# Kernel tuning notes

Measured on AMD Instinct MI355X. Metric: run time of the kernel, lower is better.

## Reference

```python
import jax, jax.numpy as jnp
import numpy as np

MOMENTUM = 0.9
BN_EPS = 1e-5
NORM_EPS = 1e-12
NUM_CLASSES = 10000
DIM_MLP = 512
NUM_EXPERTS = 3
FEAT_DIM = 256
N = 4096


def _l2norm(x, axis=-1):
    # F.normalize: x / max(||x||, eps)
    n = jnp.sqrt(jnp.sum(x * x, axis=axis, keepdims=True))
    return x / jnp.maximum(n, NORM_EPS)


def setup_inputs() -> dict:
    key = jax.random.key(0)
    ks = jax.random.split(key, 8)
    feat_in = jax.random.normal(ks[0], (N, DIM_MLP * NUM_EXPERTS), dtype=jnp.float32)
    label = jax.random.randint(ks[1], (N,), 0, NUM_CLASSES, dtype=jnp.int32)
    # encoder params
    W1 = jax.random.normal(ks[2], (DIM_MLP * NUM_EXPERTS, DIM_MLP), dtype=jnp.float32) / np.sqrt(DIM_MLP * NUM_EXPERTS)
    b1 = jnp.zeros((DIM_MLP,), dtype=jnp.float32)
    gamma = jnp.ones((DIM_MLP,), dtype=jnp.float32)
    beta = jnp.zeros((DIM_MLP,), dtype=jnp.float32)
    W2 = jax.random.normal(ks[3], (DIM_MLP, FEAT_DIM), dtype=jnp.float32) / np.sqrt(DIM_MLP)
    b2 = jnp.zeros((FEAT_DIM,), dtype=jnp.float32)
    # memory bank buffer: randn then row-normalized (as in __init__)
    memory_pt = _l2norm(jax.random.normal(ks[4], (NUM_CLASSES, FEAT_DIM), dtype=jnp.float32))
    return {"feat_in": feat_in, "label": label, "W1": W1, "b1": b1,
            "gamma": gamma, "beta": beta, "W2": W2, "b2": b2,
            "memory_pt": memory_pt}


def _encoder(feat_in, W1, b1, gamma, beta, W2, b2):
    h = feat_in @ W1 + b1                       # [N, dim_mlp]
    # BatchNorm1d in training mode: batch statistics (biased variance)
    mu = jnp.mean(h, axis=0)
    var = jnp.mean((h - mu) ** 2, axis=0)
    h = (h - mu) * jax.lax.rsqrt(var + BN_EPS) * gamma + beta
    h = jax.nn.relu(h)
    out = h @ W2 + b2                           # [N, 256]
    return _l2norm(out, axis=1)


def _update_memory(memory_pt, feat, label):
    # Strictly sequential per-sample momentum update (order matters for
    # duplicate labels), each touched row renormalized — lax.scan recurrence.
    def step(mem, xy):
        x, y = xy
        pt = MOMENTUM * mem[y] + (1.0 - MOMENTUM) * x
        pt = _l2norm(pt, axis=0)
        return mem.at[y].set(pt), None
    mem, _ = jax.lax.scan(step, memory_pt, (feat, label))
    return mem


def reference(feat_in, label, W1, b1, gamma, beta, W2, b2, memory_pt):
    feat = _encoder(feat_in, W1, b1, gamma, beta, W2, b2)   # [N, 256], unit rows
    # memory_pt.detach(): no grad flows through the memory bank
    mem = _update_memory(jax.lax.stop_gradient(memory_pt),
                         jax.lax.stop_gradient(feat), label)
    mem = jax.lax.stop_gradient(mem)
    sim_logit = jnp.einsum('nc,kc->nk', feat, mem)          # [N, K]
    return sim_logit
```

## Files before the change

### kernel.cpp

```cpp
#include <hip/hip_runtime.h>
#include <stdint.h>

typedef _Float16 f16;
typedef _Float16 f16x2 __attribute__((ext_vector_type(2)));
typedef _Float16 f16x4 __attribute__((ext_vector_type(4)));
typedef _Float16 f16x8 __attribute__((ext_vector_type(8)));
typedef float f32x4 __attribute__((ext_vector_type(4)));

typedef __attribute__((address_space(1))) void gvoid;
typedef __attribute__((address_space(3))) void lvoid;

#define NROWS 4096
#define DIMIN 1536
#define DMLP 512
#define FDIM 256
#define NCLS 10000
#define NPAD 10112
#define NBMW 320

__device__ __forceinline__ void load_lds16(const void* g, void* l) {
    __builtin_amdgcn_global_load_lds((gvoid*)g, (lvoid*)l, 16, 0, 0);
}

template<int TM, int TN, bool STATS, bool NT>
__global__ __launch_bounds__(256) void gemm_t(
    const f16* __restrict__ A, const f16* __restrict__ Bt,
    float* __restrict__ C, const float* __restrict__ bias,
    int K, int ldc, int Nstore,
    float* __restrict__ sums, float* __restrict__ sqs)
{
    constexpr int BK = 64;
    constexpr int AM = TM / 32;
    constexpr int AN = TN / 32;
    constexpr int CA = TM * 8;
    constexpr int CB = TN * 8;
    constexpr int RTOT = (CA + CB) / 256;
    constexpr int SPAN = (TM + TN) * BK;
    static_assert(CA % 256 == 0, "A/B staging split must be round-aligned");

    __shared__ f16 smem[2 * SPAN];

    const int tid  = threadIdx.x;
    const int lane = tid & 63;
    const int w    = tid >> 6;
    const int wm   = (w >> 1) * (TM / 2);
    const int wn   = (w & 1) * (TN / 2);
    const int row0 = blockIdx.x * TM;
    const int col0 = blockIdx.y * TN;
    const int quad = lane >> 4;
    const int r16  = lane & 15;

    f32x4 acc[AM][AN] = {};

    const f16* gsrc[RTOT];
    int ldsoff[RTOT];
#pragma unroll
    for (int r = 0; r < RTOT; ++r) {
        int c = tid + r * 256;
        bool isA = (c < CA);
        int cc = isA ? c : c - CA;
        int row = cc >> 3;
        int gs = (cc & 7) ^ (row & 7);
        gsrc[r] = (isA ? A + (size_t)(row0 + row) * K
                       : Bt + (size_t)(col0 + row) * K) + gs * 8;
        ldsoff[r] = (isA ? 0 : TM * BK) + cc * 8;
    }

    const int nt = K / BK;

#pragma unroll
    for (int r = 0; r < RTOT; ++r)
        load_lds16(gsrc[r], smem + ldsoff[r]);
    __syncthreads();

    int buf = 0;
    for (int t = 0; t < nt; ++t) {
        if (t + 1 < nt) {
            const int k0 = (t + 1) * BK;
            const int o = (buf ^ 1) * SPAN;
#pragma unroll
            for (int r = 0; r < RTOT; ++r)
                load_lds16(gsrc[r] + k0, smem + o + ldsoff[r]);
        }
        const f16* As = smem + buf * SPAN;
        const f16* Bs = As + TM * BK;
#pragma unroll
        for (int ks = 0; ks < 2; ++ks) {
            f16x8 af[AM], bq[AN];
#pragma unroll
            for (int mi = 0; mi < AM; ++mi) {
                int row = wm + mi * 16 + r16;
                int slot = (ks * 4 + quad) ^ (r16 & 7);
                af[mi] = *(const f16x8*)&As[row * BK + slot * 8];
            }
#pragma unroll
            for (int ni = 0; ni < AN; ++ni) {
                int row = wn + ni * 16 + r16;
                int slot = (ks * 4 + quad) ^ (r16 & 7);
                bq[ni] = *(const f16x8*)&Bs[row * BK + slot * 8];
            }
#pragma unroll
            for (int mi = 0; mi < AM; ++mi)
#pragma unroll
                for (int ni = 0; ni < AN; ++ni)
                    acc[mi][ni] = __builtin_amdgcn_mfma_f32_16x16x32_f16(
                        af[mi], bq[ni], acc[mi][ni], 0, 0, 0);
        }
        __syncthreads();
        buf ^= 1;
    }

#pragma unroll
    for (int ni = 0; ni < AN; ++ni) {
        int col = col0 + wn + ni * 16 + r16;
        float bv = bias ? bias[col] : 0.0f;
        float s = 0.0f, q = 0.0f;
        if (col < Nstore) {
#pragma unroll
            for (int mi = 0; mi < AM; ++mi) {
                int rowb = row0 + wm + mi * 16 + quad * 4;
#pragma unroll
                for (int r = 0; r < 4; ++r) {
                    float v = acc[mi][ni][r] + bv;
                    if constexpr (NT)
                        __builtin_nontemporal_store(v, &C[(size_t)(rowb + r) * ldc + col]);
                    else
                        C[(size_t)(rowb + r) * ldc + col] = v;
                    if constexpr (STATS) { s += v; q += v * v; }
                }
            }
        }
        if constexpr (STATS) {
            s += __shfl_xor(s, 16); s += __shfl_xor(s, 32);
            q += __shfl_xor(q, 16); q += __shfl_xor(q, 32);
            if (quad == 0) {
                atomicAdd(&sums[col], s);
                atomicAdd(&sqs[col], q);
            }
        }
    }
}

__global__ void zero_k(float* __restrict__ p, int n) {
    int i = blockIdx.x * 256 + threadIdx.x;
    if (i < n) p[i] = 0.0f;
}

__global__ void f32_to_f16_k(const float* __restrict__ in, f16* __restrict__ out, int n4) {
    int i = blockIdx.x * 256 + threadIdx.x;
    if (i >= n4) return;
    float4 v = *(const float4*)&in[(size_t)i * 4];
    f16x4 o = {(f16)v.x, (f16)v.y, (f16)v.z, (f16)v.w};
    *(f16x4*)&out[(size_t)i * 4] = o;
}

__global__ void transpose_f16_tile_k(const float* __restrict__ in, f16* __restrict__ out,
                                     int R, int C) {
    __shared__ float t[32][33];
    int tx = threadIdx.x & 31, ty = threadIdx.x >> 5;
    int c0 = blockIdx.x * 32, r0 = blockIdx.y * 32;
#pragma unroll
    for (int k = 0; k < 4; ++k)
        t[ty + k * 8][tx] = in[(size_t)(r0 + ty + k * 8) * C + c0 + tx];
    __syncthreads();
#pragma unroll
    for (int k = 0; k < 4; ++k)
        out[(size_t)(c0 + ty + k * 8) * R + r0 + tx] = (f16)t[tx][ty + k * 8];
}

__global__ void touch_k(const int* __restrict__ label, unsigned int* __restrict__ bm) {
    int i = blockIdx.x * 256 + threadIdx.x;
    int y = label[i];
    atomicOr(&bm[y >> 5], 1u << (y & 31));
}

__global__ void bn_finish_k(const float* __restrict__ sums, const float* __restrict__ sqs,
                            const float* __restrict__ gamma, const float* __restrict__ beta,
                            float* __restrict__ scale, float* __restrict__ shift) {
    int c = blockIdx.x * 256 + threadIdx.x;
    if (c >= DMLP) return;
    const float inv_n = 1.0f / 4096.0f;
    float mu = sums[c] * inv_n;
    float var = fmaxf(sqs[c] * inv_n - mu * mu, 0.0f);
    float a = rsqrtf(var + 1e-5f) * gamma[c];
    scale[c] = a;
    shift[c] = beta[c] - mu * a;
}

__global__ void bn_apply_k(const float* __restrict__ h, const float* __restrict__ scale,
                           const float* __restrict__ shift, f16* __restrict__ out) {
    int i = blockIdx.x * 256 + threadIdx.x;
    int c = (i & 127) * 4;
    float4 v = *(const float4*)&h[(size_t)i * 4];
    float4 sc = *(const float4*)&scale[c];
    float4 sh = *(const float4*)&shift[c];
    f16x4 o = {(f16)fmaxf(v.x * sc.x + sh.x, 0.0f),
               (f16)fmaxf(v.y * sc.y + sh.y, 0.0f),
               (f16)fmaxf(v.z * sc.z + sh.z, 0.0f),
               (f16)fmaxf(v.w * sc.w + sh.w, 0.0f)};
    *(f16x4*)&out[(size_t)i * 4] = o;
}

__global__ void l2norm_k(const float* __restrict__ X, float* __restrict__ Y, f16* __restrict__ Yh) {
    int wv = (blockIdx.x * 256 + threadIdx.x) >> 6;
    int lane = threadIdx.x & 63;
    float4 v = *(const float4*)&X[(size_t)wv * FDIM + lane * 4];
    float s = v.x * v.x + v.y * v.y + v.z * v.z + v.w * v.w;
#pragma unroll
    for (int off = 32; off > 0; off >>= 1) s += __shfl_xor(s, off);
    float inv = 1.0f / fmaxf(sqrtf(s), 1e-12f);
    float4 o = {v.x * inv, v.y * inv, v.z * inv, v.w * inv};
    *(float4*)&Y[(size_t)wv * FDIM + lane * 4] = o;
    f16x4 oh = {(f16)o.x, (f16)o.y, (f16)o.z, (f16)o.w};
    *(f16x4*)&Yh[(size_t)wv * FDIM + lane * 4] = oh;
}

__global__ void chain_k(const int* __restrict__ label, const float* __restrict__ feat,
                        const float* __restrict__ mp, const unsigned int* __restrict__ bm,
                        f16* __restrict__ memh) {
    int y = (blockIdx.x * 256 + threadIdx.x) >> 6;
    int lane = threadIdx.x & 63;
    float4 m = {0.f, 0.f, 0.f, 0.f};
    if (y < NCLS) {
        m = *(const float4*)&mp[(size_t)y * FDIM + lane * 4];
        if ((bm[y >> 5] >> (y & 31)) & 1u) {
            for (int g = 0; g < 64; ++g) {
                int lab = label[g * 64 + lane];
                unsigned long long mask = __ballot(lab == y);
                while (mask) {
                    int b = __builtin_ctzll(mask);
                    mask &= mask - 1;
                    int i = g * 64 + b;
                    float4 x = *(const float4*)&feat[(size_t)i * FDIM + lane * 4];
                    m.x = 0.9f * m.x + 0.1f * x.x;
                    m.y = 0.9f * m.y + 0.1f * x.y;
                    m.z = 0.9f * m.z + 0.1f * x.z;
                    m.w = 0.9f * m.w + 0.1f * x.w;
                    float s = m.x * m.x + m.y * m.y + m.z * m.z + m.w * m.w;
#pragma unroll
                    for (int off = 32; off > 0; off >>= 1) s += __shfl_xor(s, off);
                    float inv = 1.0f / fmaxf(sqrtf(s), 1e-12f);
                    m.x *= inv; m.y *= inv; m.z *= inv; m.w *= inv;
                }
            }
        }
    }
    f16x4 o = {(f16)m.x, (f16)m.y, (f16)m.z, (f16)m.w};
    *(f16x4*)&memh[(size_t)y * FDIM + lane * 4] = o;
}

extern "C" void kernel_launch(void* const* d_in, const int* in_sizes, int n_in,
                              void* d_out, int out_size, void* d_ws, size_t ws_size,
                              hipStream_t stream) {
    const float* feat_in = (const float*)d_in[0];
    const int*   label   = (const int*)d_in[1];
    const float* W1      = (const float*)d_in[2];
    const float* b1      = (const float*)d_in[3];
    const float* gamma   = (const float*)d_in[4];
    const float* beta    = (const float*)d_in[5];
    const float* W2      = (const float*)d_in[6];
    const float* b2      = (const float*)d_in[7];
    const float* mp      = (const float*)d_in[8];
    float* out = (float*)d_out;

    char* w = (char*)d_ws;
    f16* A1h   = (f16*)w;   w += (size_t)NROWS * DIMIN * 2;
    f16* W1t   = (f16*)w;   w += (size_t)DMLP * DIMIN * 2;
    f16* W2t   = (f16*)w;   w += (size_t)FDIM * DMLP * 2;
    float* h   = (float*)w; w += (size_t)NROWS * DMLP * 4;
    f16* h2    = (f16*)w;   w += (size_t)NROWS * DMLP * 2;
    float* out2= (float*)w; w += (size_t)NROWS * FDIM * 4;
    float* feat= (float*)w; w += (size_t)NROWS * FDIM * 4;
    f16* feath = (f16*)w;   w += (size_t)NROWS * FDIM * 2;
    f16* memh  = (f16*)w;   w += (size_t)NPAD * FDIM * 2;
    float* sums= (float*)w; w += DMLP * 4;
    float* sqs = (float*)w; w += DMLP * 4;
    unsigned int* bm = (unsigned int*)w; w += NBMW * 4;
    float* bnsc= (float*)w; w += DMLP * 4;
    float* bnsh= (float*)w; w += DMLP * 4;

    zero_k<<<6, 256, 0, stream>>>(sums, 2 * DMLP + NBMW);
    touch_k<<<NROWS / 256, 256, 0, stream>>>(label, bm);
    f32_to_f16_k<<<(NROWS * DIMIN / 4) / 256, 256, 0, stream>>>(feat_in, A1h, NROWS * DIMIN / 4);
    {
        dim3 g1(DMLP / 32, DIMIN / 32);
        transpose_f16_tile_k<<<g1, 256, 0, stream>>>(W1, W1t, DIMIN, DMLP);
        dim3 g2(FDIM / 32, DMLP / 32);
        transpose_f16_tile_k<<<g2, 256, 0, stream>>>(W2, W2t, DMLP, FDIM);
    }

    {
        dim3 g(NROWS / 128, DMLP / 64);
        gemm_t<128, 64, true, false><<<g, 256, 0, stream>>>(
            A1h, W1t, h, b1, DIMIN, DMLP, DMLP, sums, sqs);
    }

    bn_finish_k<<<2, 256, 0, stream>>>(sums, sqs, gamma, beta, bnsc, bnsh);
    bn_apply_k<<<(NROWS * DMLP / 4) / 256, 256, 0, stream>>>(h, bnsc, bnsh, h2);

    {
        dim3 g(NROWS / 64, FDIM / 64);
        gemm_t<64, 64, false, false><<<g, 256, 0, stream>>>(
            h2, W2t, out2, b2, DMLP, FDIM, FDIM, nullptr, nullptr);
    }

    l2norm_k<<<NROWS / 4, 256, 0, stream>>>(out2, feat, feath);

    chain_k<<<NPAD / 4, 256, 0, stream>>>(label, feat, mp, bm, memh);

    {
        dim3 g(NROWS / 128, NPAD / 128);
        gemm_t<128, 128, false, true><<<g, 256, 0, stream>>>(
            feath, memh, out, nullptr, FDIM, NCLS, NCLS, nullptr, nullptr);
    }
}
```

Measured before the change: 295.1 us.

## Fuse BN-apply, second GEMM and L2 normalization into one kernel; merge prep kernels

Replaces the separate bn_apply, second GEMM and l2norm kernels with a single kernel. It applies the BN scale/shift and ReLU while staging A tiles into LDS, computes a full 256-column row tile, and row-normalizes in the epilogue through a cross-wave LDS reduction. This removes the round trips through the h2 and out2 intermediates and two launches. Zeroing and the label bitmap are also merged into one single-block prep kernel that uses an LDS bitmap. The fused GEMM launches only 64 blocks, so occupancy on a large GPU is low.

```diff
diff --git a/kernel.cpp b/kernel.cpp
--- a/kernel.cpp
+++ b/kernel.cpp
@@ -141,9 +141,229 @@
     }
 }
 
-__global__ void zero_k(float* __restrict__ p, int n) {
-    int i = blockIdx.x * 256 + threadIdx.x;
-    if (i < n) p[i] = 0.0f;
+__global__ __launch_bounds__(256) void gemm2_fused_k(
+    const float* __restrict__ h, const float* __restrict__ bnsc,
+    const float* __restrict__ bnsh, const f16* __restrict__ W2t,
+    const float* __restrict__ b2,
+    float* __restrict__ feat, f16* __restrict__ feath)
+{
+    constexpr int BK = 64, TM = 64, TN = 256;
+    constexpr int AM = 2, AN = 8;
+    constexpr int SPAN = (TM + TN) * BK;
+    constexpr int RB = TN * 8 / 256;
+
+    __shared__ f16 smem[2 * SPAN];
+    __shared__ float red[2][TM];
+
+    const int tid  = threadIdx.x;
+    const int lane = tid & 63;
+    const int w    = tid >> 6;
+    const int wm   = (w >> 1) * 32;
+    const int wn   = (w & 1) * 128;
+    const int row0 = blockIdx.x * TM;
+    const int quad = lane >> 4;
+    const int r16  = lane & 15;
+
+    const int arow = tid >> 2;
+    const int ak   = (tid & 3) * 16;
+    const int aslot0 = ((tid * 2) & 7) ^ (arow & 7);
+    const float* hrow = h + (size_t)(row0 + arow) * DMLP + ak;
+
+    const f16* gsrcB[RB];
+    int ldsoffB[RB];
+#pragma unroll
+    for (int r = 0; r < RB; ++r) {
+        int cc = tid + r * 256;
+        int row = cc >> 3;
+        int gs = (cc & 7) ^ (row & 7);
+        gsrcB[r] = W2t + (size_t)row * DMLP + gs * 8;
+        ldsoffB[r] = TM * BK + cc * 8;
+    }
+
+    f32x4 acc[AM][AN] = {};
+    const int nt = DMLP / BK;
+
+    auto stageA = [&](int k0, int bufo) {
+        float4 v0 = *(const float4*)&hrow[k0];
+        float4 v1 = *(const float4*)&hrow[k0 + 4];
+        float4 v2 = *(const float4*)&hrow[k0 + 8];
+        float4 v3 = *(const float4*)&hrow[k0 + 12];
+        float4 sc0 = *(const float4*)&bnsc[k0 + ak];
+        float4 sc1 = *(const float4*)&bnsc[k0 + ak + 4];
+        float4 sc2 = *(const float4*)&bnsc[k0 + ak + 8];
+        float4 sc3 = *(const float4*)&bnsc[k0 + ak + 12];
+        float4 sh0 = *(const float4*)&bnsh[k0 + ak];
+        float4 sh1 = *(const float4*)&bnsh[k0 + ak + 4];
+        float4 sh2 = *(const float4*)&bnsh[k0 + ak + 8];
+        float4 sh3 = *(const float4*)&bnsh[k0 + ak + 12];
+        f16x8 c0 = {(f16)fmaxf(v0.x * sc0.x + sh0.x, 0.f),
+                    (f16)fmaxf(v0.y * sc0.y + sh0.y, 0.f),
+                    (f16)fmaxf(v0.z * sc0.z + sh0.z, 0.f),
+                    (f16)fmaxf(v0.w * sc0.w + sh0.w, 0.f),
+                    (f16)fmaxf(v1.x * sc1.x + sh1.x, 0.f),
+                    (f16)fmaxf(v1.y * sc1.y + sh1.y, 0.f),
+                    (f16)fmaxf(v1.z * sc1.z + sh1.z, 0.f),
+                    (f16)fmaxf(v1.w * sc1.w + sh1.w, 0.f)};
+        f16x8 c1 = {(f16)fmaxf(v2.x * sc2.x + sh2.x, 0.f),
+                    (f16)fmaxf(v2.y * sc2.y + sh2.y, 0.f),
+                    (f16)fmaxf(v2.z * sc2.z + sh2.z, 0.f),
+                    (f16)fmaxf(v2.w * sc2.w + sh2.w, 0.f),
+                    (f16)fmaxf(v3.x * sc3.x + sh3.x, 0.f),
+                    (f16)fmaxf(v3.y * sc3.y + sh3.y, 0.f),
+                    (f16)fmaxf(v3.z * sc3.z + sh3.z, 0.f),
+                    (f16)fmaxf(v3.w * sc3.w + sh3.w, 0.f)};
+        f16* As = smem + bufo;
+        *(f16x8*)&As[arow * BK + aslot0 * 8] = c0;
+        *(f16x8*)&As[arow * BK + (aslot0 ^ 1) * 8] = c1;
+    };
+
+#pragma unroll
+    for (int r = 0; r < RB; ++r)
+        load_lds16(gsrcB[r], smem + ldsoffB[r]);
+    stageA(0, 0);
+    __syncthreads();
+
+    int buf = 0;
+    for (int t = 0; t < nt; ++t) {
+        float4 n0, n1, n2, n3;
+        if (t + 1 < nt) {
+            const int k0 = (t + 1) * BK;
+            const int o = (buf ^ 1) * SPAN;
+#pragma unroll
+            for (int r = 0; r < RB; ++r)
+                load_lds16(gsrcB[r] + k0, smem + o + ldsoffB[r]);
+            n0 = *(const float4*)&hrow[k0];
+            n1 = *(const float4*)&hrow[k0 + 4];
+            n2 = *(const float4*)&hrow[k0 + 8];
+            n3 = *(const float4*)&hrow[k0 + 12];
+        }
+        const f16* As = smem + buf * SPAN;
+        const f16* Bs = As + TM * BK;
+#pragma unroll
+        for (int ks = 0; ks < 2; ++ks) {
+            f16x8 af[AM], bq[AN];
+#pragma unroll
+            for (int mi = 0; mi < AM; ++mi) {
+                int row = wm + mi * 16 + r16;
+                int slot = (ks * 4 + quad) ^ (r16 & 7);
+                af[mi] = *(const f16x8*)&As[row * BK + slot * 8];
+            }
+#pragma unroll
+            for (int ni = 0; ni < AN; ++ni) {
+                int row = wn + ni * 16 + r16;
+                int slot = (ks * 4 + quad) ^ (r16 & 7);
+                bq[ni] = *(const f16x8*)&Bs[row * BK + slot * 8];
+            }
+#pragma unroll
+            for (int mi = 0; mi < AM; ++mi)
+#pragma unroll
+                for (int ni = 0; ni < AN; ++ni)
+                    acc[mi][ni] = __builtin_amdgcn_mfma_f32_16x16x32_f16(
+                        af[mi], bq[ni], acc[mi][ni], 0, 0, 0);
+        }
+        if (t + 1 < nt) {
+            const int k0 = (t + 1) * BK;
+            const int o = (buf ^ 1) * SPAN;
+            float4 sc0 = *(const float4*)&bnsc[k0 + ak];
+            float4 sc1 = *(const float4*)&bnsc[k0 + ak + 4];
+            float4 sc2 = *(const float4*)&bnsc[k0 + ak + 8];
+            float4 sc3 = *(const float4*)&bnsc[k0 + ak + 12];
+            float4 sh0 = *(const float4*)&bnsh[k0 + ak];
+            float4 sh1 = *(const float4*)&bnsh[k0 + ak + 4];
+            float4 sh2 = *(const float4*)&bnsh[k0 + ak + 8];
+            float4 sh3 = *(const float4*)&bnsh[k0 + ak + 12];
+            f16x8 c0 = {(f16)fmaxf(n0.x * sc0.x + sh0.x, 0.f),
+                        (f16)fmaxf(n0.y * sc0.y + sh0.y, 0.f),
+                        (f16)fmaxf(n0.z * sc0.z + sh0.z, 0.f),
+                        (f16)fmaxf(n0.w * sc0.w + sh0.w, 0.f),
+                        (f16)fmaxf(n1.x * sc1.x + sh1.x, 0.f),
+                        (f16)fmaxf(n1.y * sc1.y + sh1.y, 0.f),
+                        (f16)fmaxf(n1.z * sc1.z + sh1.z, 0.f),
+                        (f16)fmaxf(n1.w * sc1.w + sh1.w, 0.f)};
+            f16x8 c1 = {(f16)fmaxf(n2.x * sc2.x + sh2.x, 0.f),
+                        (f16)fmaxf(n2.y * sc2.y + sh2.y, 0.f),
+                        (f16)fmaxf(n2.z * sc2.z + sh2.z, 0.f),
+                        (f16)fmaxf(n2.w * sc2.w + sh2.w, 0.f),
+                        (f16)fmaxf(n3.x * sc3.x + sh3.x, 0.f),
+                        (f16)fmaxf(n3.y * sc3.y + sh3.y, 0.f),
+                        (f16)fmaxf(n3.z * sc3.z + sh3.z, 0.f),
+                        (f16)fmaxf(n3.w * sc3.w + sh3.w, 0.f)};
+            f16* Asn = smem + o;
+            *(f16x8*)&Asn[arow * BK + aslot0 * 8] = c0;
+            *(f16x8*)&Asn[arow * BK + (aslot0 ^ 1) * 8] = c1;
+        }
+        __syncthreads();
+        buf ^= 1;
+    }
+
+    float ssq[AM][4] = {};
+#pragma unroll
+    for (int ni = 0; ni < AN; ++ni) {
+        int col = wn + ni * 16 + r16;
+        float bv = b2[col];
+#pragma unroll
+        for (int mi = 0; mi < AM; ++mi)
+#pragma unroll
+            for (int r = 0; r < 4; ++r) {
+                float v = acc[mi][ni][r] + bv;
+                acc[mi][ni][r] = v;
+                ssq[mi][r] += v * v;
+            }
+    }
+#pragma unroll
+    for (int mi = 0; mi < AM; ++mi)
+#pragma unroll
+        for (int r = 0; r < 4; ++r) {
+            float s = ssq[mi][r];
+            s += __shfl_xor(s, 1); s += __shfl_xor(s, 2);
+            s += __shfl_xor(s, 4); s += __shfl_xor(s, 8);
+            ssq[mi][r] = s;
+        }
+    if (r16 == 0) {
+#pragma unroll
+        for (int mi = 0; mi < AM; ++mi)
+#pragma unroll
+            for (int r = 0; r < 4; ++r)
+                red[w & 1][wm + mi * 16 + quad * 4 + r] = ssq[mi][r];
+    }
+    __syncthreads();
+    float inv[AM][4];
+#pragma unroll
+    for (int mi = 0; mi < AM; ++mi)
+#pragma unroll
+        for (int r = 0; r < 4; ++r) {
+            int rl = wm + mi * 16 + quad * 4 + r;
+            float s = red[0][rl] + red[1][rl];
+            inv[mi][r] = 1.0f / fmaxf(sqrtf(s), 1e-12f);
+        }
+#pragma unroll
+    for (int ni = 0; ni < AN; ++ni) {
+        int col = wn + ni * 16 + r16;
+#pragma unroll
+        for (int mi = 0; mi < AM; ++mi)
+#pragma unroll
+            for (int r = 0; r < 4; ++r) {
+                int row = row0 + wm + mi * 16 + quad * 4 + r;
+                float o = acc[mi][ni][r] * inv[mi][r];
+                feat[(size_t)row * FDIM + col] = o;
+                feath[(size_t)row * FDIM + col] = (f16)o;
+            }
+    }
+}
+
+__global__ void prep_k(const int* __restrict__ label, float* __restrict__ stats,
+                       unsigned int* __restrict__ bm) {
+    __shared__ unsigned int lbm[NBMW];
+    int t = threadIdx.x;
+    for (int i = t; i < NBMW; i += 256) lbm[i] = 0u;
+    for (int i = t; i < 2 * DMLP; i += 256) stats[i] = 0.0f;
+    __syncthreads();
+    for (int i = t; i < NROWS; i += 256) {
+        int y = label[i];
+        atomicOr(&lbm[y >> 5], 1u << (y & 31));
+    }
+    __syncthreads();
+    for (int i = t; i < NBMW; i += 256) bm[i] = lbm[i];
 }
 
 __global__ void f32_to_f16_k(const float* __restrict__ in, f16* __restrict__ out, int n4) {
@@ -166,12 +386,6 @@
 #pragma unroll
     for (int k = 0; k < 4; ++k)
         out[(size_t)(c0 + ty + k * 8) * R + r0 + tx] = (f16)t[tx][ty + k * 8];
-}
-
-__global__ void touch_k(const int* __restrict__ label, unsigned int* __restrict__ bm) {
-    int i = blockIdx.x * 256 + threadIdx.x;
-    int y = label[i];
-    atomicOr(&bm[y >> 5], 1u << (y & 31));
 }
 
 __global__ void bn_finish_k(const float* __restrict__ sums, const float* __restrict__ sqs,
@@ -185,34 +399,6 @@
     float a = rsqrtf(var + 1e-5f) * gamma[c];
     scale[c] = a;
     shift[c] = beta[c] - mu * a;
-}
-
-__global__ void bn_apply_k(const float* __restrict__ h, const float* __restrict__ scale,
-                           const float* __restrict__ shift, f16* __restrict__ out) {
-    int i = blockIdx.x * 256 + threadIdx.x;
-    int c = (i & 127) * 4;
-    float4 v = *(const float4*)&h[(size_t)i * 4];
-    float4 sc = *(const float4*)&scale[c];
-    float4 sh = *(const float4*)&shift[c];
-    f16x4 o = {(f16)fmaxf(v.x * sc.x + sh.x, 0.0f),
-               (f16)fmaxf(v.y * sc.y + sh.y, 0.0f),
-               (f16)fmaxf(v.z * sc.z + sh.z, 0.0f),
-               (f16)fmaxf(v.w * sc.w + sh.w, 0.0f)};
-    *(f16x4*)&out[(size_t)i * 4] = o;
-}
-
-__global__ void l2norm_k(const float* __restrict__ X, float* __restrict__ Y, f16* __restrict__ Yh) {
-    int wv = (blockIdx.x * 256 + threadIdx.x) >> 6;
-    int lane = threadIdx.x & 63;
-    float4 v = *(const float4*)&X[(size_t)wv * FDIM + lane * 4];
-    float s = v.x * v.x + v.y * v.y + v.z * v.z + v.w * v.w;
-#pragma unroll
-    for (int off = 32; off > 0; off >>= 1) s += __shfl_xor(s, off);
-    float inv = 1.0f / fmaxf(sqrtf(s), 1e-12f);
-    float4 o = {v.x * inv, v.y * inv, v.z * inv, v.w * inv};
-    *(float4*)&Y[(size_t)wv * FDIM + lane * 4] = o;
-    f16x4 oh = {(f16)o.x, (f16)o.y, (f16)o.z, (f16)o.w};
-    *(f16x4*)&Yh[(size_t)wv * FDIM + lane * 4] = oh;
 }
 
 __global__ void chain_k(const int* __restrict__ label, const float* __restrict__ feat,
@@ -268,8 +454,6 @@
     f16* W1t   = (f16*)w;   w += (size_t)DMLP * DIMIN * 2;
     f16* W2t   = (f16*)w;   w += (size_t)FDIM * DMLP * 2;
     float* h   = (float*)w; w += (size_t)NROWS * DMLP * 4;
-    f16* h2    = (f16*)w;   w += (size_t)NROWS * DMLP * 2;
-    float* out2= (float*)w; w += (size_t)NROWS * FDIM * 4;
     float* feat= (float*)w; w += (size_t)NROWS * FDIM * 4;
     f16* feath = (f16*)w;   w += (size_t)NROWS * FDIM * 2;
     f16* memh  = (f16*)w;   w += (size_t)NPAD * FDIM * 2;
@@ -279,8 +463,7 @@
     float* bnsc= (float*)w; w += DMLP * 4;
     float* bnsh= (float*)w; w += DMLP * 4;
 
-    zero_k<<<6, 256, 0, stream>>>(sums, 2 * DMLP + NBMW);
-    touch_k<<<NROWS / 256, 256, 0, stream>>>(label, bm);
+    prep_k<<<1, 256, 0, stream>>>(label, sums, bm);
     f32_to_f16_k<<<(NROWS * DIMIN / 4) / 256, 256, 0, stream>>>(feat_in, A1h, NROWS * DIMIN / 4);
     {
         dim3 g1(DMLP / 32, DIMIN / 32);
@@ -296,15 +479,8 @@
     }
 
     bn_finish_k<<<2, 256, 0, stream>>>(sums, sqs, gamma, beta, bnsc, bnsh);
-    bn_apply_k<<<(NROWS * DMLP / 4) / 256, 256, 0, stream>>>(h, bnsc, bnsh, h2);
-
-    {
-        dim3 g(NROWS / 64, FDIM / 64);
-        gemm_t<64, 64, false, false><<<g, 256, 0, stream>>>(
-            h2, W2t, out2, b2, DMLP, FDIM, FDIM, nullptr, nullptr);
-    }
-
-    l2norm_k<<<NROWS / 4, 256, 0, stream>>>(out2, feat, feath);
+
+    gemm2_fused_k<<<NROWS / 64, 256, 0, stream>>>(h, bnsc, bnsh, W2t, b2, feat, feath);
 
     chain_k<<<NPAD / 4, 256, 0, stream>>>(label, feat, mp, bm, memh);
 
```

Result: slower. 306.6 us (+3.9%).

## Fuse f32-to-f16 conversion and BN apply into GEMM A-loads; merge prep kernels

Applied to the files above, without the earlier changes.

Adds a GEMM variant that reads fp32 A directly, converts to fp16 (optionally applying BN scale/shift and ReLU) while staging into LDS. This removes the separate feat_in conversion pass and the bn_apply pass along with their intermediate buffers. The zero and label-bitmap kernels are also merged into one single-block prep kernel. The cost is that A is now loaded through registers instead of direct-to-LDS, at twice the bytes per element, and the grid is remapped with a hardcoded block swizzle.

```diff
diff --git a/kernel.cpp b/kernel.cpp
--- a/kernel.cpp
+++ b/kernel.cpp
@@ -2,7 +2,6 @@
 #include <stdint.h>
 
 typedef _Float16 f16;
-typedef _Float16 f16x2 __attribute__((ext_vector_type(2)));
 typedef _Float16 f16x4 __attribute__((ext_vector_type(4)));
 typedef _Float16 f16x8 __attribute__((ext_vector_type(8)));
 typedef float f32x4 __attribute__((ext_vector_type(4)));
@@ -141,17 +140,178 @@
     }
 }
 
-__global__ void zero_k(float* __restrict__ p, int n) {
-    int i = blockIdx.x * 256 + threadIdx.x;
-    if (i < n) p[i] = 0.0f;
-}
-
-__global__ void f32_to_f16_k(const float* __restrict__ in, f16* __restrict__ out, int n4) {
-    int i = blockIdx.x * 256 + threadIdx.x;
-    if (i >= n4) return;
-    float4 v = *(const float4*)&in[(size_t)i * 4];
-    f16x4 o = {(f16)v.x, (f16)v.y, (f16)v.z, (f16)v.w};
-    *(f16x4*)&out[(size_t)i * 4] = o;
+template<int TN, bool BNA, bool STATS>
+__global__ __launch_bounds__(256) void gemm_f32a_t(
+    const float* __restrict__ Af, const f16* __restrict__ Bt,
+    const float* __restrict__ sc, const float* __restrict__ sh,
+    float* __restrict__ C, const float* __restrict__ bias,
+    int K, int ldc,
+    float* __restrict__ sums, float* __restrict__ sqs)
+{
+    constexpr int TM = 64, BK = 64;
+    constexpr int AM = TM / 32;
+    constexpr int AN = TN / 32;
+    constexpr int RA = TM * 8 / 256;
+    constexpr int RB = TN * 8 / 256;
+    constexpr int SPAN = (TM + TN) * BK;
+
+    __shared__ f16 smem[2 * SPAN];
+
+    const int tid  = threadIdx.x;
+    const int lane = tid & 63;
+    const int w    = tid >> 6;
+    const int wm   = (w >> 1) * (TM / 2);
+    const int wn   = (w & 1) * (TN / 2);
+    const int lin  = blockIdx.x;
+    const int bx   = (lin & 7) * 8 + (lin >> 5);
+    const int by   = (lin >> 3) & 3;
+    const int row0 = bx * TM;
+    const int col0 = by * TN;
+    const int quad = lane >> 4;
+    const int r16  = lane & 15;
+
+    f32x4 acc[AM][AN] = {};
+
+    const float* asrc[RA];
+    int ag8[RA], adst[RA];
+#pragma unroll
+    for (int r = 0; r < RA; ++r) {
+        int cc = tid + r * 256;
+        int row = cc >> 3, g = cc & 7;
+        asrc[r] = Af + (size_t)(row0 + row) * K + g * 8;
+        ag8[r]  = g * 8;
+        adst[r] = row * BK + (g ^ (row & 7)) * 8;
+    }
+    const f16* gsrcB[RB];
+    int ldsoffB[RB];
+#pragma unroll
+    for (int r = 0; r < RB; ++r) {
+        int cc = tid + r * 256;
+        int row = cc >> 3, g = cc & 7;
+        gsrcB[r] = Bt + (size_t)(col0 + row) * K + (g ^ (row & 7)) * 8;
+        ldsoffB[r] = TM * BK + cc * 8;
+    }
+
+    auto xform = [&](float4 a, float4 b, int k) -> f16x8 {
+        if constexpr (BNA) {
+            float4 s0 = *(const float4*)&sc[k], s1 = *(const float4*)&sc[k + 4];
+            float4 h0 = *(const float4*)&sh[k], h1 = *(const float4*)&sh[k + 4];
+            return f16x8{(f16)fmaxf(a.x * s0.x + h0.x, 0.f),
+                         (f16)fmaxf(a.y * s0.y + h0.y, 0.f),
+                         (f16)fmaxf(a.z * s0.z + h0.z, 0.f),
+                         (f16)fmaxf(a.w * s0.w + h0.w, 0.f),
+                         (f16)fmaxf(b.x * s1.x + h1.x, 0.f),
+                         (f16)fmaxf(b.y * s1.y + h1.y, 0.f),
+                         (f16)fmaxf(b.z * s1.z + h1.z, 0.f),
+                         (f16)fmaxf(b.w * s1.w + h1.w, 0.f)};
+        } else {
+            return f16x8{(f16)a.x, (f16)a.y, (f16)a.z, (f16)a.w,
+                         (f16)b.x, (f16)b.y, (f16)b.z, (f16)b.w};
+        }
+    };
+
+    const int nt = K / BK;
+
+#pragma unroll
+    for (int r = 0; r < RB; ++r)
+        load_lds16(gsrcB[r], smem + ldsoffB[r]);
+#pragma unroll
+    for (int r = 0; r < RA; ++r) {
+        float4 a = *(const float4*)(asrc[r]);
+        float4 b = *(const float4*)(asrc[r] + 4);
+        *(f16x8*)&smem[adst[r]] = xform(a, b, ag8[r]);
+    }
+    __syncthreads();
+
+    int buf = 0;
+    for (int t = 0; t < nt; ++t) {
+        float4 na[RA], nb[RA];
+        if (t + 1 < nt) {
+            const int k0n = (t + 1) * BK;
+            const int o = (buf ^ 1) * SPAN;
+#pragma unroll
+            for (int r = 0; r < RB; ++r)
+                load_lds16(gsrcB[r] + k0n, smem + o + ldsoffB[r]);
+#pragma unroll
+            for (int r = 0; r < RA; ++r) {
+                na[r] = *(const float4*)(asrc[r] + k0n);
+                nb[r] = *(const float4*)(asrc[r] + k0n + 4);
+            }
+        }
+        const f16* As = smem + buf * SPAN;
+        const f16* Bs = As + TM * BK;
+#pragma unroll
+        for (int ks = 0; ks < 2; ++ks) {
+            f16x8 af[AM], bq[AN];
+#pragma unroll
+            for (int mi = 0; mi < AM; ++mi) {
+                int row = wm + mi * 16 + r16;
+                int slot = (ks * 4 + quad) ^ (r16 & 7);
+                af[mi] = *(const f16x8*)&As[row * BK + slot * 8];
+            }
+#pragma unroll
+            for (int ni = 0; ni < AN; ++ni) {
+                int row = wn + ni * 16 + r16;
+                int slot = (ks * 4 + quad) ^ (r16 & 7);
+                bq[ni] = *(const f16x8*)&Bs[row * BK + slot * 8];
+            }
+#pragma unroll
+            for (int mi = 0; mi < AM; ++mi)
+#pragma unroll
+                for (int ni = 0; ni < AN; ++ni)
+                    acc[mi][ni] = __builtin_amdgcn_mfma_f32_16x16x32_f16(
+                        af[mi], bq[ni], acc[mi][ni], 0, 0, 0);
+        }
+        if (t + 1 < nt) {
+            const int k0n = (t + 1) * BK;
+            f16* Ad = smem + (buf ^ 1) * SPAN;
+#pragma unroll
+            for (int r = 0; r < RA; ++r)
+                *(f16x8*)&Ad[adst[r]] = xform(na[r], nb[r], k0n + ag8[r]);
+        }
+        __syncthreads();
+        buf ^= 1;
+    }
+
+#pragma unroll
+    for (int ni = 0; ni < AN; ++ni) {
+        int col = col0 + wn + ni * 16 + r16;
+        float bv = bias[col];
+        float s = 0.0f, q = 0.0f;
+#pragma unroll
+        for (int mi = 0; mi < AM; ++mi) {
+            int rowb = row0 + wm + mi * 16 + quad * 4;
+#pragma unroll
+            for (int r = 0; r < 4; ++r) {
+                float v = acc[mi][ni][r] + bv;
+                C[(size_t)(rowb + r) * ldc + col] = v;
+                if constexpr (STATS) { s += v; q += v * v; }
+            }
+        }
+        if constexpr (STATS) {
+            s += __shfl_xor(s, 16); s += __shfl_xor(s, 32);
+            q += __shfl_xor(q, 16); q += __shfl_xor(q, 32);
+            if (quad == 0) {
+                atomicAdd(&sums[col], s);
+                atomicAdd(&sqs[col], q);
+            }
+        }
+    }
+}
+
+__global__ void prep_k(const int* __restrict__ label, float* __restrict__ stats,
+                       unsigned int* __restrict__ bm) {
+    __shared__ unsigned int lbm[NBMW];
+    int t = threadIdx.x;
+    for (int i = t; i < NBMW; i += 256) lbm[i] = 0u;
+    for (int i = t; i < 2 * DMLP; i += 256) stats[i] = 0.0f;
+    __syncthreads();
+    for (int i = t; i < NROWS; i += 256) {
+        int y = label[i];
+        atomicOr(&lbm[y >> 5], 1u << (y & 31));
+    }
+    __syncthreads();
+    for (int i = t; i < NBMW; i += 256) bm[i] = lbm[i];
 }
 
 __global__ void transpose_f16_tile_k(const float* __restrict__ in, f16* __restrict__ out,
@@ -166,12 +326,6 @@
 #pragma unroll
     for (int k = 0; k < 4; ++k)
         out[(size_t)(c0 + ty + k * 8) * R + r0 + tx] = (f16)t[tx][ty + k * 8];
-}
-
-__global__ void touch_k(const int* __restrict__ label, unsigned int* __restrict__ bm) {
-    int i = blockIdx.x * 256 + threadIdx.x;
-    int y = label[i];
-    atomicOr(&bm[y >> 5], 1u << (y & 31));
 }
 
 __global__ void bn_finish_k(const float* __restrict__ sums, const float* __restrict__ sqs,
@@ -185,20 +339,6 @@
     float a = rsqrtf(var + 1e-5f) * gamma[c];
     scale[c] = a;
     shift[c] = beta[c] - mu * a;
-}
-
-__global__ void bn_apply_k(const float* __restrict__ h, const float* __restrict__ scale,
-                           const float* __restrict__ shift, f16* __restrict__ out) {
-    int i = blockIdx.x * 256 + threadIdx.x;
-    int c = (i & 127) * 4;
-    float4 v = *(const float4*)&h[(size_t)i * 4];
-    float4 sc = *(const float4*)&scale[c];
-    float4 sh = *(const float4*)&shift[c];
-    f16x4 o = {(f16)fmaxf(v.x * sc.x + sh.x, 0.0f),
-               (f16)fmaxf(v.y * sc.y + sh.y, 0.0f),
-               (f16)fmaxf(v.z * sc.z + sh.z, 0.0f),
-               (f16)fmaxf(v.w * sc.w + sh.w, 0.0f)};
-    *(f16x4*)&out[(size_t)i * 4] = o;
 }
 
 __global__ void l2norm_k(const float* __restrict__ X, float* __restrict__ Y, f16* __restrict__ Yh) {
@@ -264,11 +404,9 @@
     float* out = (float*)d_out;
 
     char* w = (char*)d_ws;
-    f16* A1h   = (f16*)w;   w += (size_t)NROWS * DIMIN * 2;
     f16* W1t   = (f16*)w;   w += (size_t)DMLP * DIMIN * 2;
     f16* W2t   = (f16*)w;   w += (size_t)FDIM * DMLP * 2;
     float* h   = (float*)w; w += (size_t)NROWS * DMLP * 4;
-    f16* h2    = (f16*)w;   w += (size_t)NROWS * DMLP * 2;
     float* out2= (float*)w; w += (size_t)NROWS * FDIM * 4;
     float* feat= (float*)w; w += (size_t)NROWS * FDIM * 4;
     f16* feath = (f16*)w;   w += (size_t)NROWS * FDIM * 2;
@@ -279,9 +417,7 @@
     float* bnsc= (float*)w; w += DMLP * 4;
     float* bnsh= (float*)w; w += DMLP * 4;
 
-    zero_k<<<6, 256, 0, stream>>>(sums, 2 * DMLP + NBMW);
-    touch_k<<<NROWS / 256, 256, 0, stream>>>(label, bm);
-    f32_to_f16_k<<<(NROWS * DIMIN / 4) / 256, 256, 0, stream>>>(feat_in, A1h, NROWS * DIMIN / 4);
+    prep_k<<<1, 256, 0, stream>>>(label, sums, bm);
     {
         dim3 g1(DMLP / 32, DIMIN / 32);
         transpose_f16_tile_k<<<g1, 256, 0, stream>>>(W1, W1t, DIMIN, DMLP);
@@ -289,20 +425,13 @@
         transpose_f16_tile_k<<<g2, 256, 0, stream>>>(W2, W2t, DMLP, FDIM);
     }
 
-    {
-        dim3 g(NROWS / 128, DMLP / 64);
-        gemm_t<128, 64, true, false><<<g, 256, 0, stream>>>(
-            A1h, W1t, h, b1, DIMIN, DMLP, DMLP, sums, sqs);
-    }
+    gemm_f32a_t<128, false, true><<<256, 256, 0, stream>>>(
+        feat_in, W1t, nullptr, nullptr, h, b1, DIMIN, DMLP, sums, sqs);
 
     bn_finish_k<<<2, 256, 0, stream>>>(sums, sqs, gamma, beta, bnsc, bnsh);
-    bn_apply_k<<<(NROWS * DMLP / 4) / 256, 256, 0, stream>>>(h, bnsc, bnsh, h2);
-
-    {
-        dim3 g(NROWS / 64, FDIM / 64);
-        gemm_t<64, 64, false, false><<<g, 256, 0, stream>>>(
-            h2, W2t, out2, b2, DMLP, FDIM, FDIM, nullptr, nullptr);
-    }
+
+    gemm_f32a_t<64, true, false><<<256, 256, 0, stream>>>(
+        h, W2t, bnsc, bnsh, out2, b2, DMLP, FDIM, nullptr, nullptr);
 
     l2norm_k<<<NROWS / 4, 256, 0, stream>>>(out2, feat, feath);
 
```

After: 305.1 us. 3.4% more time.
